# Optimization experiments

Hardware: AMD Instinct MI355X
Metric: run time of the kernel (lower is better)

## Reference

```python
import jax, jax.numpy as jnp
import numpy as np

PI = float(np.pi)

def erp_xyz_coords(h, w):
    # matches calculate_erp_coord: pixel grid -> uv -> unit-sphere xyz
    yy, xx = jnp.meshgrid(jnp.linspace(0.0, h - 1.0, h), jnp.linspace(0.0, w - 1.0, w), indexing='ij')
    u = (xx - (w / 2.0 + 0.5)) / w * 2.0 * PI
    v = (yy - (h / 2.0 + 0.5)) / h * PI
    xyz = jnp.stack([jnp.cos(v) * jnp.sin(u), jnp.sin(v), jnp.cos(v) * jnp.cos(u)], axis=-1)
    return xyz.reshape(h * w, 3)  # (HW, 3)


def setup_inputs() -> dict:
    key = jax.random.key(0)
    ks = jax.random.split(key, 16)
    B, C, H, W = 1, 128, 16, 32
    Nkv = 1280
    s = 0.02
    inp = {
        'erp_feature': jax.random.normal(ks[0], (B, C, H, W), jnp.float32),
        'ico_feature': jax.random.normal(ks[1], (B, Nkv, C), jnp.float32),
        'ico_coord': jax.random.normal(ks[2], (B, Nkv, 3), jnp.float32),
        # SA branch params (torch Linear: y = x @ W.T + b, W is (out,in))
        'Wq_sa': jax.random.normal(ks[3], (C, C), jnp.float32) * s,
        'Wkv_sa': jax.random.normal(ks[4], (2 * C, C), jnp.float32) * s,
        'proj_sa_w': jax.random.normal(ks[5], (C, C), jnp.float32) * s,
        'proj_sa_b': jnp.zeros((C,), jnp.float32),
        # DA branch params
        'Wq_da': jax.random.normal(ks[6], (C, C), jnp.float32) * s,
        'Wkv_da': jax.random.normal(ks[7], (2 * C, C), jnp.float32) * s,
        'Wdelta': jax.random.normal(ks[8], (C, 3), jnp.float32) * s,
        'proj_da_w': jax.random.normal(ks[9], (C, C), jnp.float32) * s,
        'proj_da_b': jnp.zeros((C,), jnp.float32),
        # gates
        'gate_sa_w': jax.random.normal(ks[10], (C, 2 * C), jnp.float32) * s,
        'gate_da_w': jax.random.normal(ks[11], (C, 2 * C), jnp.float32) * s,
    }
    return inp


def _forward(erp_feature, ico_feature, ico_coord,
             Wq_sa, Wkv_sa, proj_sa_w, proj_sa_b,
             Wq_da, Wkv_da, Wdelta, proj_da_w, proj_da_b,
             gate_sa_w, gate_da_w):
    B, C, H, W = erp_feature.shape
    Nq = H * W
    q = erp_feature.reshape(B, C, Nq).transpose(0, 2, 1)  # (B, Nq, C)
    qc = erp_xyz_coords(H, W)[None]                        # (1, Nq, 3) broadcasts over B

    # ---- SA branch (iteration = 1) ----
    q_sa = q @ Wq_sa.T                                     # (B, Nq, C)
    kv_sa = (ico_feature @ Wkv_sa.T).reshape(B, -1, 2, C)
    k_sa, v_sa = kv_sa[:, :, 0], kv_sa[:, :, 1]
    attn_sa = jax.nn.softmax(jnp.einsum('bqc,bkc->bqk', q_sa, k_sa) * (C ** -0.5), axis=-1)
    out_sa = jnp.einsum('bqk,bkc->bqc', attn_sa, v_sa)
    # faithful to torch: .transpose(1,2).reshape(B, Nq, C) scrambles layout
    out_sa = out_sa.transpose(0, 2, 1).reshape(B, Nq, C)
    sa = out_sa @ proj_sa_w.T + proj_sa_b

    # ---- DA branch (iteration = 1) ----
    q_da = q @ Wq_da.T
    kv_da = (ico_feature @ Wkv_da.T).reshape(B, -1, 2, C)
    k_da, v_da = kv_da[:, :, 0], kv_da[:, :, 1]
    # feature affinity: sum_c exp(-|q_c - k_c|)   -> (B, Nq, Nkv)
    feat_aff = jnp.exp(-jnp.abs(q_da[:, :, None, :] - k_da[:, None, :, :])).sum(-1)
    # positional term: (exp(-|dq - dk|) @ Wdelta.T).sum(-1) == exp(...) . Wdelta.sum(0)
    pos_exp = jnp.exp(-jnp.abs(qc[:, :, None, :] - ico_coord[:, None, :, :]))  # (B,Nq,Nkv,3)
    pos_aff = jnp.einsum('bqkt,t->bqk', pos_exp, Wdelta.sum(0))
    attn_da = jax.nn.softmax((feat_aff + pos_aff) * (1.0 / C), axis=-1)
    out_da = jnp.einsum('bqk,bkc->bqc', attn_da, v_da)
    da = out_da @ proj_da_w.T + proj_da_b

    # ---- gated fusion ----
    cat = jnp.concatenate([sa, da], axis=-1)               # (B, Nq, 2C)
    sa_factor = jax.nn.sigmoid(cat @ gate_sa_w.T)
    da_factor = jax.nn.sigmoid(cat @ gate_da_w.T)
    fused = sa_factor * sa + da_factor * da                # (B, Nq, C)
    return fused.reshape(B, H, W, C).transpose(0, 3, 1, 2)  # (B, C, H, W)


def reference(erp_feature, ico_feature, ico_coord,
              Wq_sa, Wkv_sa, proj_sa_w, proj_sa_b,
              Wq_da, Wkv_da, Wdelta, proj_da_w, proj_da_b,
              gate_sa_w, gate_da_w):
    return _forward(erp_feature, ico_feature, ico_coord,
                    Wq_sa, Wkv_sa, proj_sa_w, proj_sa_b,
                    Wq_da, Wkv_da, Wdelta, proj_da_w, proj_da_b,
                    gate_sa_w, gate_da_w)
```

## Files before the change

kernel.cpp:

```cpp
#include <hip/hip_runtime.h>
#include <math.h>

#define NQ   512
#define NKV  1280
#define CDIM 128

#define OFF_WDSUM 0
#define OFF_SUMS  16
#define OFF_QSA   1056
#define OFF_QDA   66592
#define OFF_KSAT  132128
#define OFF_VSA   295968
#define OFF_KDAT  459808
#define OFF_VDA   623648
#define OFF_OUT   787488

__global__ __launch_bounds__(256) void prep_kernel(
    const float* __restrict__ erp, const float* __restrict__ ico,
    const float* __restrict__ wq_sa, const float* __restrict__ wq_da,
    const float* __restrict__ wkv_sa, const float* __restrict__ wkv_da,
    const float* __restrict__ wdelta, float* __restrict__ ws)
{
  int bx = blockIdx.x, t = threadIdx.x;
  if (bx < 320) {
    __shared__ float x4[4 * CDIM];
    int k0 = bx * 4;
    for (int i = t; i < 512; i += 256) {
      int ky = i >> 7, j = i & 127;
      x4[j * 4 + ky] = ico[(k0 + ky) * CDIM + j];
    }
    __syncthreads();
    const float4* wsa4 = (const float4*)(wkv_sa + t * CDIM);
    const float4* wda4 = (const float4*)(wkv_da + t * CDIM);
    float as0=0,as1=0,as2=0,as3=0, ad0=0,ad1=0,ad2=0,ad3=0;
    #pragma unroll 4
    for (int j4 = 0; j4 < 32; ++j4) {
      float4 wsv = wsa4[j4];
      float4 wdv = wda4[j4];
      float4 x0 = *(const float4*)&x4[(j4 * 4 + 0) * 4];
      float4 x1 = *(const float4*)&x4[(j4 * 4 + 1) * 4];
      float4 x2 = *(const float4*)&x4[(j4 * 4 + 2) * 4];
      float4 x3 = *(const float4*)&x4[(j4 * 4 + 3) * 4];
      as0 = fmaf(wsv.x, x0.x, as0); as1 = fmaf(wsv.x, x0.y, as1);
      as2 = fmaf(wsv.x, x0.z, as2); as3 = fmaf(wsv.x, x0.w, as3);
      ad0 = fmaf(wdv.x, x0.x, ad0); ad1 = fmaf(wdv.x, x0.y, ad1);
      ad2 = fmaf(wdv.x, x0.z, ad2); ad3 = fmaf(wdv.x, x0.w, ad3);
      as0 = fmaf(wsv.y, x1.x, as0); as1 = fmaf(wsv.y, x1.y, as1);
      as2 = fmaf(wsv.y, x1.z, as2); as3 = fmaf(wsv.y, x1.w, as3);
      ad0 = fmaf(wdv.y, x1.x, ad0); ad1 = fmaf(wdv.y, x1.y, ad1);
      ad2 = fmaf(wdv.y, x1.z, ad2); ad3 = fmaf(wdv.y, x1.w, ad3);
      as0 = fmaf(wsv.z, x2.x, as0); as1 = fmaf(wsv.z, x2.y, as1);
      as2 = fmaf(wsv.z, x2.z, as2); as3 = fmaf(wsv.z, x2.w, as3);
      ad0 = fmaf(wdv.z, x2.x, ad0); ad1 = fmaf(wdv.z, x2.y, ad1);
      ad2 = fmaf(wdv.z, x2.z, ad2); ad3 = fmaf(wdv.z, x2.w, ad3);
      as0 = fmaf(wsv.w, x3.x, as0); as1 = fmaf(wsv.w, x3.y, as1);
      as2 = fmaf(wsv.w, x3.z, as2); as3 = fmaf(wsv.w, x3.w, as3);
      ad0 = fmaf(wdv.w, x3.x, ad0); ad1 = fmaf(wdv.w, x3.y, ad1);
      ad2 = fmaf(wdv.w, x3.z, ad2); ad3 = fmaf(wdv.w, x3.w, ad3);
    }
    if (t < 128) {
      *(float4*)(ws + OFF_KSAT + t * NKV + k0) = make_float4(as0, as1, as2, as3);
      *(float4*)(ws + OFF_KDAT + t * NKV + k0) = make_float4(ad0, ad1, ad2, ad3);
    } else {
      int c = t - 128;
      ws[OFF_VSA + (k0 + 0) * CDIM + c] = as0;
      ws[OFF_VSA + (k0 + 1) * CDIM + c] = as1;
      ws[OFF_VSA + (k0 + 2) * CDIM + c] = as2;
      ws[OFF_VSA + (k0 + 3) * CDIM + c] = as3;
      ws[OFF_VDA + (k0 + 0) * CDIM + c] = ad0;
      ws[OFF_VDA + (k0 + 1) * CDIM + c] = ad1;
      ws[OFF_VDA + (k0 + 2) * CDIM + c] = ad2;
      ws[OFF_VDA + (k0 + 3) * CDIM + c] = ad3;
    }
  } else if (bx < 448) {
    __shared__ float q4[4 * CDIM];
    int n0 = (bx - 320) * 4;
    for (int i = t; i < 512; i += 256)
      q4[i] = erp[(i >> 2) * NQ + n0 + (i & 3)];
    __syncthreads();
    const float* w = (t < 128) ? wq_sa : wq_da;
    int c = t & 127;
    const float4* w4 = (const float4*)(w + c * CDIM);
    float a0 = 0.f, a1 = 0.f, a2 = 0.f, a3 = 0.f;
    #pragma unroll 8
    for (int j4 = 0; j4 < 32; ++j4) {
      float4 wv = w4[j4];
      float4 q0 = *(const float4*)&q4[(j4 * 4 + 0) * 4];
      float4 q1 = *(const float4*)&q4[(j4 * 4 + 1) * 4];
      float4 q2 = *(const float4*)&q4[(j4 * 4 + 2) * 4];
      float4 q3 = *(const float4*)&q4[(j4 * 4 + 3) * 4];
      a0 = fmaf(wv.x, q0.x, a0); a1 = fmaf(wv.x, q0.y, a1);
      a2 = fmaf(wv.x, q0.z, a2); a3 = fmaf(wv.x, q0.w, a3);
      a0 = fmaf(wv.y, q1.x, a0); a1 = fmaf(wv.y, q1.y, a1);
      a2 = fmaf(wv.y, q1.z, a2); a3 = fmaf(wv.y, q1.w, a3);
      a0 = fmaf(wv.z, q2.x, a0); a1 = fmaf(wv.z, q2.y, a1);
      a2 = fmaf(wv.z, q2.z, a2); a3 = fmaf(wv.z, q2.w, a3);
      a0 = fmaf(wv.w, q3.x, a0); a1 = fmaf(wv.w, q3.y, a1);
      a2 = fmaf(wv.w, q3.z, a2); a3 = fmaf(wv.w, q3.w, a3);
    }
    float* o = ws + ((t < 128) ? OFF_QSA : OFF_QDA);
    o[(n0 + 0) * CDIM + c] = a0;
    o[(n0 + 1) * CDIM + c] = a1;
    o[(n0 + 2) * CDIM + c] = a2;
    o[(n0 + 3) * CDIM + c] = a3;
  } else if (bx == 448) {
    *(float4*)(ws + OFF_SUMS + t * 4) = make_float4(0.f, 0.f, 0.f, 0.f);
    if (t < 3) {
      float s = 0.f;
      for (int i = 0; i < 128; ++i) s += wdelta[i * 3 + t];
      ws[OFF_WDSUM + t] = s;
    }
  } else {
    int base = OFF_OUT + (bx - 449) * 1024 + t * 4;
    *(float4*)(ws + base) = make_float4(0.f, 0.f, 0.f, 0.f);
  }
}

__global__ __launch_bounds__(256) void attn_kernel(
    const float* __restrict__ coord, float* __restrict__ ws)
{
  __shared__ __align__(16) float qjf[4 * CDIM];
  __shared__ __align__(16) float psc[2][4][128];
  __shared__ __align__(16) float posk[4][128];
  __shared__ __align__(16) float se[4][128];
  __shared__ float red[2][4];
  __shared__ float qcr[4][3];
  __shared__ float wdl[3];
  int b = blockIdx.x, t = threadIdx.x;
  int br = (b < 1280) ? 1 : 0;
  int bb = br ? b : b - 1280;
  int g = bb / 10, z = bb - g * 10;
  int n0 = g * 4, k0 = z * 128;

  const float* qsrc = ws + (br ? OFF_QDA : OFF_QSA);
  for (int i = t; i < 512; i += 256) {
    int r = i & 3, j = i >> 2;
    qjf[j * 4 + r] = qsrc[(n0 + r) * CDIM + j];
  }
  if (br) {
    if (t < 4) {
      int n = n0 + t;
      float x = (float)(n & 31), y = (float)(n >> 5);
      float u  = (x - 16.5f) * 0.19634954084936207f;
      float vv = (y -  8.5f) * 0.19634954084936207f;
      float cv = cosf(vv);
      qcr[t][0] = cv * sinf(u);
      qcr[t][1] = sinf(vv);
      qcr[t][2] = cv * cosf(u);
    }
    if (t >= 64 && t < 67) wdl[t - 64] = ws[OFF_WDSUM + t - 64];
  }
  __syncthreads();

  int kl = t & 127, jh = t >> 7;
  int k = k0 + kl;
  {
    const float* kp = ws + (br ? OFF_KDAT : OFF_KSAT) + k + jh * 64 * NKV;
    const float4* qj = (const float4*)&qjf[jh * 64 * 4];
    float a0 = 0.f, a1 = 0.f, a2 = 0.f, a3 = 0.f;
    if (br) {
      #pragma unroll 4
      for (int j = 0; j < 64; ++j) {
        float kv = kp[j * NKV];
        float4 q = qj[j];
        a0 += __expf(-fabsf(q.x - kv)); a1 += __expf(-fabsf(q.y - kv));
        a2 += __expf(-fabsf(q.z - kv)); a3 += __expf(-fabsf(q.w - kv));
      }
    } else {
      #pragma unroll 8
      for (int j = 0; j < 64; ++j) {
        float kv = kp[j * NKV];
        float4 q = qj[j];
        a0 = fmaf(q.x, kv, a0); a1 = fmaf(q.y, kv, a1);
        a2 = fmaf(q.z, kv, a2); a3 = fmaf(q.w, kv, a3);
      }
    }
    psc[jh][0][kl] = a0; psc[jh][1][kl] = a1;
    psc[jh][2][kl] = a2; psc[jh][3][kl] = a3;
    if (br && jh == 1) {
      float c0 = coord[k * 3], c1 = coord[k * 3 + 1], c2 = coord[k * 3 + 2];
      float w0 = wdl[0], w1 = wdl[1], w2 = wdl[2];
      #pragma unroll
      for (int r = 0; r < 4; ++r)
        posk[r][kl] = w0 * __expf(-fabsf(qcr[r][0] - c0))
                    + w1 * __expf(-fabsf(qcr[r][1] - c1))
                    + w2 * __expf(-fabsf(qcr[r][2] - c2));
    }
  }
  __syncthreads();

  if (t < 128) {
    const float scl = 0.088388347648318447f;
    const float i128 = 0.0078125f;
    float s[4];
    #pragma unroll
    for (int r = 0; r < 4; ++r) {
      float tot = psc[0][r][t] + psc[1][r][t];
      float l = br ? (tot + posk[r][t]) * i128 : tot * scl;
      float e = __expf(l);
      se[r][t] = e;
      s[r] = e;
    }
    #pragma unroll
    for (int o = 32; o > 0; o >>= 1) {
      s[0] += __shfl_down(s[0], o, 64); s[1] += __shfl_down(s[1], o, 64);
      s[2] += __shfl_down(s[2], o, 64); s[3] += __shfl_down(s[3], o, 64);
    }
    if ((t & 63) == 0) {
      int w = t >> 6;
      red[w][0] = s[0]; red[w][1] = s[1]; red[w][2] = s[2]; red[w][3] = s[3];
    }
  }
  __syncthreads();
  if (t < 4)
    atomicAdd(ws + OFF_SUMS + br * 512 + n0 + t, red[0][t] + red[1][t]);

  int c = t & 127, h = t >> 7;
  const float* vp = ws + (br ? OFF_VDA : OFF_VSA) + k0 * CDIM + c;
  float acc0 = 0.f, acc1 = 0.f;
  #pragma unroll 4
  for (int ko = 0; ko < 128; ko += 4) {
    float4 pa = *(const float4*)&se[h][ko];
    float4 pb = *(const float4*)&se[h + 2][ko];
    float v0 = vp[(ko + 0) * CDIM];
    float v1 = vp[(ko + 1) * CDIM];
    float v2 = vp[(ko + 2) * CDIM];
    float v3 = vp[(ko + 3) * CDIM];
    acc0 = fmaf(pa.x, v0, acc0); acc1 = fmaf(pb.x, v0, acc1);
    acc0 = fmaf(pa.y, v1, acc0); acc1 = fmaf(pb.y, v1, acc1);
    acc0 = fmaf(pa.z, v2, acc0); acc1 = fmaf(pb.z, v2, acc1);
    acc0 = fmaf(pa.w, v3, acc0); acc1 = fmaf(pb.w, v3, acc1);
  }
  float* op = ws + OFF_OUT + br * (NQ * CDIM);
  atomicAdd(op + (n0 + h) * CDIM + c,     acc0);
  atomicAdd(op + (n0 + h + 2) * CDIM + c, acc1);
}

__global__ __launch_bounds__(256) void finalize_kernel(
    const float* __restrict__ psa, const float* __restrict__ bsa,
    const float* __restrict__ pda, const float* __restrict__ bda,
    const float* __restrict__ gsa, const float* __restrict__ gda,
    float* __restrict__ out, float* __restrict__ ws)
{
  __shared__ float sain[2][CDIM];
  __shared__ float dain[2][CDIM];
  __shared__ float cat[2][2 * CDIM];
  __shared__ float gl[2][2][CDIM];
  int i0 = blockIdx.x * 2, t = threadIdx.x;
  int h = t >> 7, c = t & 127;
  #pragma unroll
  for (int rr = 0; rr < 2; ++rr) {
    int i = i0 + rr;
    if (h == 0) {
      int row = (i & 3) * 128 + c;
      float s = ws[OFF_SUMS + row];
      sain[rr][c] = ws[OFF_OUT + row * CDIM + (i >> 2)] / s;
    } else {
      float s = ws[OFF_SUMS + 512 + i];
      dain[rr][c] = ws[OFF_OUT + NQ * CDIM + i * CDIM + c] / s;
    }
  }
  __syncthreads();
  {
    const float4* w4 = (const float4*)((h ? pda : psa) + c * CDIM);
    const float* in0 = h ? dain[0] : sain[0];
    const float* in1 = h ? dain[1] : sain[1];
    float a0 = 0, a1 = 0, b0 = 0, b1 = 0;
    #pragma unroll 8
    for (int j4 = 0; j4 < 32; ++j4) {
      float4 wv = w4[j4];
      float4 x0 = *(const float4*)&in0[j4 * 4];
      float4 x1 = *(const float4*)&in1[j4 * 4];
      a0 = fmaf(wv.x, x0.x, a0); a1 = fmaf(wv.y, x0.y, a1);
      a0 = fmaf(wv.z, x0.z, a0); a1 = fmaf(wv.w, x0.w, a1);
      b0 = fmaf(wv.x, x1.x, b0); b1 = fmaf(wv.y, x1.y, b1);
      b0 = fmaf(wv.z, x1.z, b0); b1 = fmaf(wv.w, x1.w, b1);
    }
    float bias = h ? bda[c] : bsa[c];
    cat[0][h * CDIM + c] = bias + a0 + a1;
    cat[1][h * CDIM + c] = bias + b0 + b1;
  }
  __syncthreads();
  {
    const float4* g4 = (const float4*)((h ? gda : gsa) + c * 2 * CDIM);
    float a0 = 0, a1 = 0, b0 = 0, b1 = 0;
    #pragma unroll 8
    for (int j4 = 0; j4 < 64; ++j4) {
      float4 gv = g4[j4];
      float4 c0 = *(const float4*)&cat[0][j4 * 4];
      float4 c1 = *(const float4*)&cat[1][j4 * 4];
      a0 = fmaf(gv.x, c0.x, a0); a1 = fmaf(gv.y, c0.y, a1);
      a0 = fmaf(gv.z, c0.z, a0); a1 = fmaf(gv.w, c0.w, a1);
      b0 = fmaf(gv.x, c1.x, b0); b1 = fmaf(gv.y, c1.y, b1);
      b0 = fmaf(gv.z, c1.z, b0); b1 = fmaf(gv.w, c1.w, b1);
    }
    gl[0][h][c] = 1.0f / (1.0f + __expf(-(a0 + a1)));
    gl[1][h][c] = 1.0f / (1.0f + __expf(-(b0 + b1)));
  }
  __syncthreads();
  {
    int i = i0 + h;
    out[c * NQ + i] = gl[h][0][c] * cat[h][c] + gl[h][1][c] * cat[h][CDIM + c];
  }
}

extern "C" void kernel_launch(void* const* d_in, const int* in_sizes, int n_in,
                              void* d_out, int out_size, void* d_ws, size_t ws_size,
                              hipStream_t stream)
{
  (void)in_sizes; (void)n_in; (void)out_size; (void)ws_size;
  const float* erp       = (const float*)d_in[0];
  const float* ico       = (const float*)d_in[1];
  const float* coord     = (const float*)d_in[2];
  const float* wq_sa     = (const float*)d_in[3];
  const float* wkv_sa    = (const float*)d_in[4];
  const float* proj_sa_w = (const float*)d_in[5];
  const float* proj_sa_b = (const float*)d_in[6];
  const float* wq_da     = (const float*)d_in[7];
  const float* wkv_da    = (const float*)d_in[8];
  const float* wdelta    = (const float*)d_in[9];
  const float* proj_da_w = (const float*)d_in[10];
  const float* proj_da_b = (const float*)d_in[11];
  const float* gate_sa   = (const float*)d_in[12];
  const float* gate_da   = (const float*)d_in[13];
  float* out = (float*)d_out;
  float* ws  = (float*)d_ws;

  hipLaunchKernelGGL(prep_kernel, dim3(577), dim3(256), 0, stream,
                     erp, ico, wq_sa, wq_da, wkv_sa, wkv_da, wdelta, ws);
  hipLaunchKernelGGL(attn_kernel, dim3(2560), dim3(256), 0, stream,
                     coord, ws);
  hipLaunchKernelGGL(finalize_kernel, dim3(256), dim3(256), 0, stream,
                     proj_sa_w, proj_sa_b, proj_da_w, proj_da_b,
                     gate_sa, gate_da, out, ws);
}
```

Measured before the change: 142.8 us.

## Process 8 queries per attention block and fold log2e scaling into exp2

The attention kernel now handles 8 query rows per block instead of 4, halving the grid and reusing each loaded key/value element across twice as many queries. The log2(e) factor is folded into the stored DA queries, keys and coordinates and into the softmax scale, so exp2f replaces __expf. The finalize kernel processes 4 rows per block instead of 2. The cost is more registers and shared memory per block and fewer blocks to spread across the GPU.

Result: slower. 152.2 us (+6.6%).

```diff
diff --git a/kernel.cpp b/kernel.cpp
--- a/kernel.cpp
+++ b/kernel.cpp
@@ -4,6 +4,7 @@
 #define NQ   512
 #define NKV  1280
 #define CDIM 128
+#define L2E  1.4426950408889634f
 
 #define OFF_WDSUM 0
 #define OFF_SUMS  16
@@ -60,7 +61,8 @@
     }
     if (t < 128) {
       *(float4*)(ws + OFF_KSAT + t * NKV + k0) = make_float4(as0, as1, as2, as3);
-      *(float4*)(ws + OFF_KDAT + t * NKV + k0) = make_float4(ad0, ad1, ad2, ad3);
+      *(float4*)(ws + OFF_KDAT + t * NKV + k0) =
+          make_float4(ad0 * L2E, ad1 * L2E, ad2 * L2E, ad3 * L2E);
     } else {
       int c = t - 128;
       ws[OFF_VSA + (k0 + 0) * CDIM + c] = as0;
@@ -98,11 +100,12 @@
       a0 = fmaf(wv.w, q3.x, a0); a1 = fmaf(wv.w, q3.y, a1);
       a2 = fmaf(wv.w, q3.z, a2); a3 = fmaf(wv.w, q3.w, a3);
     }
+    float sc = (t < 128) ? 1.0f : L2E;
     float* o = ws + ((t < 128) ? OFF_QSA : OFF_QDA);
-    o[(n0 + 0) * CDIM + c] = a0;
-    o[(n0 + 1) * CDIM + c] = a1;
-    o[(n0 + 2) * CDIM + c] = a2;
-    o[(n0 + 3) * CDIM + c] = a3;
+    o[(n0 + 0) * CDIM + c] = a0 * sc;
+    o[(n0 + 1) * CDIM + c] = a1 * sc;
+    o[(n0 + 2) * CDIM + c] = a2 * sc;
+    o[(n0 + 3) * CDIM + c] = a3 * sc;
   } else if (bx == 448) {
     *(float4*)(ws + OFF_SUMS + t * 4) = make_float4(0.f, 0.f, 0.f, 0.f);
     if (t < 3) {
@@ -119,34 +122,34 @@
 __global__ __launch_bounds__(256) void attn_kernel(
     const float* __restrict__ coord, float* __restrict__ ws)
 {
-  __shared__ __align__(16) float qjf[4 * CDIM];
-  __shared__ __align__(16) float psc[2][4][128];
-  __shared__ __align__(16) float posk[4][128];
-  __shared__ __align__(16) float se[4][128];
-  __shared__ float red[2][4];
-  __shared__ float qcr[4][3];
+  __shared__ __align__(16) float qjf[8 * CDIM];
+  __shared__ __align__(16) float psc[2][8][128];
+  __shared__ __align__(16) float posk[8][128];
+  __shared__ __align__(16) float se[8][128];
+  __shared__ float red[2][8];
+  __shared__ float qcr[8][3];
   __shared__ float wdl[3];
   int b = blockIdx.x, t = threadIdx.x;
-  int br = (b < 1280) ? 1 : 0;
-  int bb = br ? b : b - 1280;
+  int br = (b < 640) ? 1 : 0;
+  int bb = br ? b : b - 640;
   int g = bb / 10, z = bb - g * 10;
-  int n0 = g * 4, k0 = z * 128;
+  int n0 = g * 8, k0 = z * 128;
 
   const float* qsrc = ws + (br ? OFF_QDA : OFF_QSA);
-  for (int i = t; i < 512; i += 256) {
-    int r = i & 3, j = i >> 2;
-    qjf[j * 4 + r] = qsrc[(n0 + r) * CDIM + j];
+  for (int i = t; i < 1024; i += 256) {
+    int r = i & 7, j = i >> 3;
+    qjf[j * 8 + r] = qsrc[(n0 + r) * CDIM + j];
   }
   if (br) {
-    if (t < 4) {
+    if (t < 8) {
       int n = n0 + t;
       float x = (float)(n & 31), y = (float)(n >> 5);
       float u  = (x - 16.5f) * 0.19634954084936207f;
       float vv = (y -  8.5f) * 0.19634954084936207f;
       float cv = cosf(vv);
-      qcr[t][0] = cv * sinf(u);
-      qcr[t][1] = sinf(vv);
-      qcr[t][2] = cv * cosf(u);
+      qcr[t][0] = cv * sinf(u) * L2E;
+      qcr[t][1] = sinf(vv) * L2E;
+      qcr[t][2] = cv * cosf(u) * L2E;
     }
     if (t >= 64 && t < 67) wdl[t - 64] = ws[OFF_WDSUM + t - 64];
   }
@@ -156,84 +159,101 @@
   int k = k0 + kl;
   {
     const float* kp = ws + (br ? OFF_KDAT : OFF_KSAT) + k + jh * 64 * NKV;
-    const float4* qj = (const float4*)&qjf[jh * 64 * 4];
-    float a0 = 0.f, a1 = 0.f, a2 = 0.f, a3 = 0.f;
+    const float4* qj = (const float4*)&qjf[jh * 64 * 8];
+    float a0=0,a1=0,a2=0,a3=0,a4=0,a5=0,a6=0,a7=0;
     if (br) {
       #pragma unroll 4
       for (int j = 0; j < 64; ++j) {
         float kv = kp[j * NKV];
-        float4 q = qj[j];
-        a0 += __expf(-fabsf(q.x - kv)); a1 += __expf(-fabsf(q.y - kv));
-        a2 += __expf(-fabsf(q.z - kv)); a3 += __expf(-fabsf(q.w - kv));
+        float4 qa = qj[j * 2], qb = qj[j * 2 + 1];
+        a0 += exp2f(-fabsf(qa.x - kv)); a1 += exp2f(-fabsf(qa.y - kv));
+        a2 += exp2f(-fabsf(qa.z - kv)); a3 += exp2f(-fabsf(qa.w - kv));
+        a4 += exp2f(-fabsf(qb.x - kv)); a5 += exp2f(-fabsf(qb.y - kv));
+        a6 += exp2f(-fabsf(qb.z - kv)); a7 += exp2f(-fabsf(qb.w - kv));
       }
     } else {
-      #pragma unroll 8
+      #pragma unroll 4
       for (int j = 0; j < 64; ++j) {
         float kv = kp[j * NKV];
-        float4 q = qj[j];
-        a0 = fmaf(q.x, kv, a0); a1 = fmaf(q.y, kv, a1);
-        a2 = fmaf(q.z, kv, a2); a3 = fmaf(q.w, kv, a3);
+        float4 qa = qj[j * 2], qb = qj[j * 2 + 1];
+        a0 = fmaf(qa.x, kv, a0); a1 = fmaf(qa.y, kv, a1);
+        a2 = fmaf(qa.z, kv, a2); a3 = fmaf(qa.w, kv, a3);
+        a4 = fmaf(qb.x, kv, a4); a5 = fmaf(qb.y, kv, a5);
+        a6 = fmaf(qb.z, kv, a6); a7 = fmaf(qb.w, kv, a7);
       }
     }
     psc[jh][0][kl] = a0; psc[jh][1][kl] = a1;
     psc[jh][2][kl] = a2; psc[jh][3][kl] = a3;
+    psc[jh][4][kl] = a4; psc[jh][5][kl] = a5;
+    psc[jh][6][kl] = a6; psc[jh][7][kl] = a7;
     if (br && jh == 1) {
-      float c0 = coord[k * 3], c1 = coord[k * 3 + 1], c2 = coord[k * 3 + 2];
+      float c0 = coord[k * 3] * L2E;
+      float c1 = coord[k * 3 + 1] * L2E;
+      float c2 = coord[k * 3 + 2] * L2E;
       float w0 = wdl[0], w1 = wdl[1], w2 = wdl[2];
       #pragma unroll
-      for (int r = 0; r < 4; ++r)
-        posk[r][kl] = w0 * __expf(-fabsf(qcr[r][0] - c0))
-                    + w1 * __expf(-fabsf(qcr[r][1] - c1))
-                    + w2 * __expf(-fabsf(qcr[r][2] - c2));
+      for (int r = 0; r < 8; ++r)
+        posk[r][kl] = w0 * exp2f(-fabsf(qcr[r][0] - c0))
+                    + w1 * exp2f(-fabsf(qcr[r][1] - c1))
+                    + w2 * exp2f(-fabsf(qcr[r][2] - c2));
     }
   }
   __syncthreads();
 
   if (t < 128) {
-    const float scl = 0.088388347648318447f;
-    const float i128 = 0.0078125f;
-    float s[4];
+    const float csa = 0.088388347648318447f * L2E;
+    const float cda = 0.0078125f * L2E;
+    float s[8];
     #pragma unroll
-    for (int r = 0; r < 4; ++r) {
+    for (int r = 0; r < 8; ++r) {
       float tot = psc[0][r][t] + psc[1][r][t];
-      float l = br ? (tot + posk[r][t]) * i128 : tot * scl;
-      float e = __expf(l);
+      float l = br ? (tot + posk[r][t]) * cda : tot * csa;
+      float e = exp2f(l);
       se[r][t] = e;
       s[r] = e;
     }
     #pragma unroll
     for (int o = 32; o > 0; o >>= 1) {
-      s[0] += __shfl_down(s[0], o, 64); s[1] += __shfl_down(s[1], o, 64);
-      s[2] += __shfl_down(s[2], o, 64); s[3] += __shfl_down(s[3], o, 64);
+      #pragma unroll
+      for (int r = 0; r < 8; ++r) s[r] += __shfl_down(s[r], o, 64);
     }
     if ((t & 63) == 0) {
       int w = t >> 6;
-      red[w][0] = s[0]; red[w][1] = s[1]; red[w][2] = s[2]; red[w][3] = s[3];
-    }
-  }
-  __syncthreads();
-  if (t < 4)
+      #pragma unroll
+      for (int r = 0; r < 8; ++r) red[w][r] = s[r];
+    }
+  }
+  __syncthreads();
+  if (t < 8)
     atomicAdd(ws + OFF_SUMS + br * 512 + n0 + t, red[0][t] + red[1][t]);
 
   int c = t & 127, h = t >> 7;
   const float* vp = ws + (br ? OFF_VDA : OFF_VSA) + k0 * CDIM + c;
-  float acc0 = 0.f, acc1 = 0.f;
+  float acc0 = 0.f, acc1 = 0.f, acc2 = 0.f, acc3 = 0.f;
   #pragma unroll 4
   for (int ko = 0; ko < 128; ko += 4) {
-    float4 pa = *(const float4*)&se[h][ko];
-    float4 pb = *(const float4*)&se[h + 2][ko];
+    float4 p0 = *(const float4*)&se[h][ko];
+    float4 p1 = *(const float4*)&se[h + 2][ko];
+    float4 p2 = *(const float4*)&se[h + 4][ko];
+    float4 p3 = *(const float4*)&se[h + 6][ko];
     float v0 = vp[(ko + 0) * CDIM];
     float v1 = vp[(ko + 1) * CDIM];
     float v2 = vp[(ko + 2) * CDIM];
     float v3 = vp[(ko + 3) * CDIM];
-    acc0 = fmaf(pa.x, v0, acc0); acc1 = fmaf(pb.x, v0, acc1);
-    acc0 = fmaf(pa.y, v1, acc0); acc1 = fmaf(pb.y, v1, acc1);
-    acc0 = fmaf(pa.z, v2, acc0); acc1 = fmaf(pb.z, v2, acc1);
-    acc0 = fmaf(pa.w, v3, acc0); acc1 = fmaf(pb.w, v3, acc1);
+    acc0 = fmaf(p0.x, v0, acc0); acc1 = fmaf(p1.x, v0, acc1);
+    acc2 = fmaf(p2.x, v0, acc2); acc3 = fmaf(p3.x, v0, acc3);
+    acc0 = fmaf(p0.y, v1, acc0); acc1 = fmaf(p1.y, v1, acc1);
+    acc2 = fmaf(p2.y, v1, acc2); acc3 = fmaf(p3.y, v1, acc3);
+    acc0 = fmaf(p0.z, v2, acc0); acc1 = fmaf(p1.z, v2, acc1);
+    acc2 = fmaf(p2.z, v2, acc2); acc3 = fmaf(p3.z, v2, acc3);
+    acc0 = fmaf(p0.w, v3, acc0); acc1 = fmaf(p1.w, v3, acc1);
+    acc2 = fmaf(p2.w, v3, acc2); acc3 = fmaf(p3.w, v3, acc3);
   }
   float* op = ws + OFF_OUT + br * (NQ * CDIM);
   atomicAdd(op + (n0 + h) * CDIM + c,     acc0);
   atomicAdd(op + (n0 + h + 2) * CDIM + c, acc1);
+  atomicAdd(op + (n0 + h + 4) * CDIM + c, acc2);
+  atomicAdd(op + (n0 + h + 6) * CDIM + c, acc3);
 }
 
 __global__ __launch_bounds__(256) void finalize_kernel(
@@ -242,14 +262,14 @@
     const float* __restrict__ gsa, const float* __restrict__ gda,
     float* __restrict__ out, float* __restrict__ ws)
 {
-  __shared__ float sain[2][CDIM];
-  __shared__ float dain[2][CDIM];
-  __shared__ float cat[2][2 * CDIM];
-  __shared__ float gl[2][2][CDIM];
-  int i0 = blockIdx.x * 2, t = threadIdx.x;
+  __shared__ float sain[4][CDIM];
+  __shared__ float dain[4][CDIM];
+  __shared__ float cat[4][2 * CDIM];
+  __shared__ float gl[4][2][CDIM];
+  int i0 = blockIdx.x * 4, t = threadIdx.x;
   int h = t >> 7, c = t & 127;
   #pragma unroll
-  for (int rr = 0; rr < 2; ++rr) {
+  for (int rr = 0; rr < 4; ++rr) {
     int i = i0 + rr;
     if (h == 0) {
       int row = (i & 3) * 128 + c;
@@ -263,44 +283,61 @@
   __syncthreads();
   {
     const float4* w4 = (const float4*)((h ? pda : psa) + c * CDIM);
-    const float* in0 = h ? dain[0] : sain[0];
-    const float* in1 = h ? dain[1] : sain[1];
-    float a0 = 0, a1 = 0, b0 = 0, b1 = 0;
-    #pragma unroll 8
+    float a0 = 0, a1 = 0, a2 = 0, a3 = 0;
+    #pragma unroll 4
     for (int j4 = 0; j4 < 32; ++j4) {
       float4 wv = w4[j4];
-      float4 x0 = *(const float4*)&in0[j4 * 4];
-      float4 x1 = *(const float4*)&in1[j4 * 4];
-      a0 = fmaf(wv.x, x0.x, a0); a1 = fmaf(wv.y, x0.y, a1);
-      a0 = fmaf(wv.z, x0.z, a0); a1 = fmaf(wv.w, x0.w, a1);
-      b0 = fmaf(wv.x, x1.x, b0); b1 = fmaf(wv.y, x1.y, b1);
-      b0 = fmaf(wv.z, x1.z, b0); b1 = fmaf(wv.w, x1.w, b1);
+      const float (*inp)[CDIM] = h ? dain : sain;
+      float4 x0 = *(const float4*)&inp[0][j4 * 4];
+      float4 x1 = *(const float4*)&inp[1][j4 * 4];
+      float4 x2 = *(const float4*)&inp[2][j4 * 4];
+      float4 x3 = *(const float4*)&inp[3][j4 * 4];
+      a0 = fmaf(wv.x, x0.x, a0); a0 = fmaf(wv.y, x0.y, a0);
+      a0 = fmaf(wv.z, x0.z, a0); a0 = fmaf(wv.w, x0.w, a0);
+      a1 = fmaf(wv.x, x1.x, a1); a1 = fmaf(wv.y, x1.y, a1);
+      a1 = fmaf(wv.z, x1.z, a1); a1 = fmaf(wv.w, x1.w, a1);
+      a2 = fmaf(wv.x, x2.x, a2); a2 = fmaf(wv.y, x2.y, a2);
+      a2 = fmaf(wv.z, x2.z, a2); a2 = fmaf(wv.w, x2.w, a2);
+      a3 = fmaf(wv.x, x3.x, a3); a3 = fmaf(wv.y, x3.y, a3);
+      a3 = fmaf(wv.z, x3.z, a3); a3 = fmaf(wv.w, x3.w, a3);
     }
     float bias = h ? bda[c] : bsa[c];
-    cat[0][h * CDIM + c] = bias + a0 + a1;
-    cat[1][h * CDIM + c] = bias + b0 + b1;
+    cat[0][h * CDIM + c] = bias + a0;
+    cat[1][h * CDIM + c] = bias + a1;
+    cat[2][h * CDIM + c] = bias + a2;
+    cat[3][h * CDIM + c] = bias + a3;
   }
   __syncthreads();
   {
     const float4* g4 = (const float4*)((h ? gda : gsa) + c * 2 * CDIM);
-    float a0 = 0, a1 = 0, b0 = 0, b1 = 0;
-    #pragma unroll 8
+    float a0 = 0, a1 = 0, a2 = 0, a3 = 0;
+    #pragma unroll 4
     for (int j4 = 0; j4 < 64; ++j4) {
       float4 gv = g4[j4];
       float4 c0 = *(const float4*)&cat[0][j4 * 4];
       float4 c1 = *(const float4*)&cat[1][j4 * 4];
-      a0 = fmaf(gv.x, c0.x, a0); a1 = fmaf(gv.y, c0.y, a1);
-      a0 = fmaf(gv.z, c0.z, a0); a1 = fmaf(gv.w, c0.w, a1);
-      b0 = fmaf(gv.x, c1.x, b0); b1 = fmaf(gv.y, c1.y, b1);
-      b0 = fmaf(gv.z, c1.z, b0); b1 = fmaf(gv.w, c1.w, b1);
-    }
-    gl[0][h][c] = 1.0f / (1.0f + __expf(-(a0 + a1)));
-    gl[1][h][c] = 1.0f / (1.0f + __expf(-(b0 + b1)));
-  }
-  __syncthreads();
-  {
-    int i = i0 + h;
-    out[c * NQ + i] = gl[h][0][c] * cat[h][c] + gl[h][1][c] * cat[h][CDIM + c];
+      float4 c2 = *(const float4*)&cat[2][j4 * 4];
+      float4 c3 = *(const float4*)&cat[3][j4 * 4];
+      a0 = fmaf(gv.x, c0.x, a0); a0 = fmaf(gv.y, c0.y, a0);
+      a0 = fmaf(gv.z, c0.z, a0); a0 = fmaf(gv.w, c0.w, a0);
+      a1 = fmaf(gv.x, c1.x, a1); a1 = fmaf(gv.y, c1.y, a1);
+      a1 = fmaf(gv.z, c1.z, a1); a1 = fmaf(gv.w, c1.w, a1);
+      a2 = fmaf(gv.x, c2.x, a2); a2 = fmaf(gv.y, c2.y, a2);
+      a2 = fmaf(gv.z, c2.z, a2); a2 = fmaf(gv.w, c2.w, a2);
+      a3 = fmaf(gv.x, c3.x, a3); a3 = fmaf(gv.y, c3.y, a3);
+      a3 = fmaf(gv.z, c3.z, a3); a3 = fmaf(gv.w, c3.w, a3);
+    }
+    gl[0][h][c] = 1.0f / (1.0f + __expf(-a0));
+    gl[1][h][c] = 1.0f / (1.0f + __expf(-a1));
+    gl[2][h][c] = 1.0f / (1.0f + __expf(-a2));
+    gl[3][h][c] = 1.0f / (1.0f + __expf(-a3));
+  }
+  __syncthreads();
+  #pragma unroll
+  for (int u = 0; u < 2; ++u) {
+    int rr = h * 2 + u;
+    int i = i0 + rr;
+    out[c * NQ + i] = gl[rr][0][c] * cat[rr][c] + gl[rr][1][c] * cat[rr][CDIM + c];
   }
 }
 
@@ -328,9 +365,9 @@
 
   hipLaunchKernelGGL(prep_kernel, dim3(577), dim3(256), 0, stream,
                      erp, ico, wq_sa, wq_da, wkv_sa, wkv_da, wdelta, ws);
-  hipLaunchKernelGGL(attn_kernel, dim3(2560), dim3(256), 0, stream,
+  hipLaunchKernelGGL(attn_kernel, dim3(1280), dim3(256), 0, stream,
                      coord, ws);
-  hipLaunchKernelGGL(finalize_kernel, dim3(256), dim3(256), 0, stream,
+  hipLaunchKernelGGL(finalize_kernel, dim3(128), dim3(256), 0, stream,
                      proj_sa_w, proj_sa_b, proj_da_w, proj_da_b,
                      gate_sa, gate_da, out, ws);
 }
```
